# Kernel tuning notes

Measured on AMD Instinct MI355X. Metric: run time of the kernel, lower is better.

Reference implementation:

```python
import jax, jax.numpy as jnp
import numpy as np

N_HEADS = 16
GROUP_SIZE = 4
D_MODEL = 2048
N_GROUPS = N_HEADS // GROUP_SIZE  # 4 KV heads
HEAD_DIM = D_MODEL // N_HEADS     # 128
B, S = 2, 2048


def setup_inputs() -> dict:
    key = jax.random.key(0)
    ks = jax.random.split(key, 10)
    sd = 1.0 / np.sqrt(D_MODEL)
    inp = {
        "x": jax.random.normal(ks[0], (B, S, D_MODEL), dtype=jnp.float32),
        # per-position, per-pair rotation angles (llama-style freqs)
        "rotary_freqs": jax.random.uniform(ks[1], (S, HEAD_DIM // 2), dtype=jnp.float32) * 6.283,
        # weights stored as [in, out] so forward is x @ W + b
        "Wq": jax.random.normal(ks[2], (D_MODEL, D_MODEL), dtype=jnp.float32) * sd,
        "bq": jnp.zeros((D_MODEL,), dtype=jnp.float32),
        "Wk": jax.random.normal(ks[3], (D_MODEL, N_GROUPS * HEAD_DIM), dtype=jnp.float32) * sd,
        "bk": jnp.zeros((N_GROUPS * HEAD_DIM,), dtype=jnp.float32),
        "Wv": jax.random.normal(ks[4], (D_MODEL, N_GROUPS * HEAD_DIM), dtype=jnp.float32) * sd,
        "bv": jnp.zeros((N_GROUPS * HEAD_DIM,), dtype=jnp.float32),
        "Wo": jax.random.normal(ks[5], (D_MODEL, D_MODEL), dtype=jnp.float32) * sd,
        "bo": jnp.zeros((D_MODEL,), dtype=jnp.float32),
    }
    return inp


def _rope(t, cos, sin):
    # t: [B, S, H, head_dim]; cos/sin: [1, S, 1, head_dim//2]
    t2 = t.reshape(t.shape[:-1] + (HEAD_DIM // 2, 2))
    te, to = t2[..., 0], t2[..., 1]
    re = te * cos - to * sin
    ro = te * sin + to * cos
    return jnp.stack([re, ro], axis=-1).reshape(t.shape)


def reference(x, rotary_freqs, Wq, bq, Wk, bk, Wv, bv, Wo, bo):
    Bx, Sx, _ = x.shape
    q = (x @ Wq + bq).reshape(Bx, Sx, N_HEADS, HEAD_DIM)
    k = (x @ Wk + bk).reshape(Bx, Sx, N_GROUPS, HEAD_DIM)
    v = (x @ Wv + bv).reshape(Bx, Sx, N_GROUPS, HEAD_DIM)

    cos = jnp.cos(rotary_freqs)[None, :, None, :]
    sin = jnp.sin(rotary_freqs)[None, :, None, :]
    q = _rope(q, cos, sin)
    k = _rope(k, cos, sin)

    q = q.transpose(0, 2, 1, 3)  # [B, H, S, hd]
    k = k.transpose(0, 2, 1, 3)  # [B, G, S, hd]
    v = v.transpose(0, 2, 1, 3)  # [B, G, S, hd]

    rep = N_HEADS // N_GROUPS
    k = jnp.repeat(k, rep, axis=1)  # repeat_interleave over head dim
    v = jnp.repeat(v, rep, axis=1)

    scores = jnp.einsum("bhsd,bhtd->bhst", q, k) / jnp.sqrt(jnp.float32(HEAD_DIM))
    att = jax.nn.softmax(scores, axis=-1)
    out = jnp.einsum("bhst,bhtd->bhsd", att, v)  # [B, H, S, hd]
    out = out.transpose(0, 2, 1, 3).reshape(Bx, Sx, D_MODEL)
    return out @ Wo + bo
```

## Files before the change

### kernel.cpp

```cpp
#include <hip/hip_runtime.h>
#include <cstdint>
#include <cstddef>

#define NB 2
#define SEQ 2048
#define DMODEL 2048
#define NHEAD 16
#define HDIM 128
#define NGRP 4
#define NKV (NGRP * HDIM)
#define NQKV (DMODEL + 2 * NKV)
#define MROWS (NB * SEQ)
#define QSCALE_LOG2E 0.12751743f

typedef unsigned short u16_t;
typedef unsigned int u32_t;
typedef __bf16 bf16x8 __attribute__((ext_vector_type(8)));
typedef __bf16 bf16x4 __attribute__((ext_vector_type(4)));
typedef float f32x4 __attribute__((ext_vector_type(4)));

static __device__ __forceinline__ u16_t f2bf(float f) {
  u32_t u = __builtin_bit_cast(u32_t, f);
  u32_t r = u + 0x7FFFu + ((u >> 16) & 1u);
  return (u16_t)(r >> 16);
}


__global__ void k_cast_x(const float* __restrict__ x, u16_t* __restrict__ xb) {
  int i = blockIdx.x * 256 + threadIdx.x;
  float4 v = ((const float4*)x)[i];
  uint2 pk;
  pk.x = (u32_t)f2bf(v.x) | ((u32_t)f2bf(v.y) << 16);
  pk.y = (u32_t)f2bf(v.z) | ((u32_t)f2bf(v.w) << 16);
  ((uint2*)xb)[i] = pk;
}

__global__ void k_tables(const float* __restrict__ rf, float* __restrict__ cosT,
                         float* __restrict__ sinT) {
  int i = blockIdx.x * 256 + threadIdx.x;
  float f = rf[i];
  cosT[i] = cosf(f);
  sinT[i] = sinf(f);
}

__global__ void k_bias(const float* __restrict__ bq, const float* __restrict__ bk,
                       const float* __restrict__ bv, float* __restrict__ bqkv) {
  int i = blockIdx.x * 256 + threadIdx.x;
  float v = (i < DMODEL) ? bq[i] : (i < DMODEL + NKV ? bk[i - DMODEL] : bv[i - DMODEL - NKV]);
  bqkv[i] = v;
}

__global__ void k_transpose_cast(const float* __restrict__ W, int N,
                                 u16_t* __restrict__ Wt, int K) {
  __shared__ float tile[64][65];
  int n0 = blockIdx.x * 64, k0 = blockIdx.y * 64;
  int t = threadIdx.x;
#pragma unroll
  for (int pass = 0; pass < 4; ++pass) {
    int slot = pass * 256 + t;
    int r = slot >> 4, c4 = (slot & 15) * 4;
    float4 v = *(const float4*)(W + (size_t)(k0 + r) * N + n0 + c4);
    tile[r][c4] = v.x; tile[r][c4 + 1] = v.y; tile[r][c4 + 2] = v.z; tile[r][c4 + 3] = v.w;
  }
  __syncthreads();
  int nr = t >> 2, seg = t & 3;
  alignas(16) u16_t o[16];
#pragma unroll
  for (int kk = 0; kk < 16; ++kk) o[kk] = f2bf(tile[seg * 16 + kk][nr]);
  u16_t* dst = Wt + (size_t)(n0 + nr) * K + k0 + seg * 16;
  ((int4*)dst)[0] = ((const int4*)o)[0];
  ((int4*)dst)[1] = ((const int4*)o)[1];
}


template <int EPI>
__global__ __launch_bounds__(256, 2) void k_gemm(
    const u16_t* __restrict__ A, const u16_t* __restrict__ Bt, const float* __restrict__ bias,
    float* __restrict__ Cout, u16_t* __restrict__ Qb, u16_t* __restrict__ Kb,
    u16_t* __restrict__ Vt, const float* __restrict__ cosT, const float* __restrict__ sinT,
    int M, int N, int K) {
  __shared__ u16_t lds[16384];
  int tid = threadIdx.x;
  int wid = tid >> 6, lane = tid & 63;
  int l15 = lane & 15, l4 = lane >> 4;
  int wrow = wid >> 1, wcol = wid & 1;

  int m0 = blockIdx.y << 7, n0 = blockIdx.x << 7;

  f32x4 acc[4][4] = {};

  auto stage = [&](int t) {
    u16_t* Al = lds + (t & 1) * 4096;
    u16_t* Bl = lds + 8192 + (t & 1) * 4096;
    int kbase = t * 32;
#pragma unroll
    for (int ss = 0; ss < 2; ++ss) {
      int slot = tid + ss * 256;
      int row = slot >> 2, c = slot & 3;
      int cs = c ^ (row & 3);
      __builtin_amdgcn_global_load_lds(
          (const __attribute__((address_space(1))) u32_t*)(A + (size_t)(m0 + row) * K + kbase + cs * 8),
          (__attribute__((address_space(3))) u32_t*)(Al + slot * 8), 16, 0, 0);
      __builtin_amdgcn_global_load_lds(
          (const __attribute__((address_space(1))) u32_t*)(Bt + (size_t)(n0 + row) * K + kbase + cs * 8),
          (__attribute__((address_space(3))) u32_t*)(Bl + slot * 8), 16, 0, 0);
    }
  };

  stage(0);
  stage(1);

  const int NT = K >> 5;
  for (int t = 0; t < NT; ++t) {
    if (t == NT - 1) {
      asm volatile("s_waitcnt vmcnt(0)" ::: "memory");
    } else {
      asm volatile("s_waitcnt vmcnt(4)" ::: "memory");
    }
    __builtin_amdgcn_s_barrier();
    __builtin_amdgcn_sched_barrier(0);

    const u16_t* Acur = lds + (t & 1) * 4096;
    const u16_t* Bcur = lds + 8192 + (t & 1) * 4096;

    int chunk = l4 ^ (l15 & 3);
    bf16x8 af[4], bfr[4];
#pragma unroll
    for (int i = 0; i < 4; ++i)
      af[i] = *(const bf16x8*)(Acur + (wrow * 64 + i * 16 + l15) * 32 + chunk * 8);
#pragma unroll
    for (int j = 0; j < 4; ++j)
      bfr[j] = *(const bf16x8*)(Bcur + (wcol * 64 + j * 16 + l15) * 32 + chunk * 8);

    __builtin_amdgcn_s_setprio(1);
#pragma unroll
    for (int i = 0; i < 4; ++i)
#pragma unroll
      for (int j = 0; j < 4; ++j)
        acc[i][j] = __builtin_amdgcn_mfma_f32_16x16x32_bf16(af[i], bfr[j], acc[i][j], 0, 0, 0);
    __builtin_amdgcn_s_setprio(0);

    __builtin_amdgcn_sched_barrier(0);
    __builtin_amdgcn_s_barrier();
    __builtin_amdgcn_sched_barrier(0);
    if (t + 2 < NT) stage(t + 2);
  }

  if (EPI == 0) {
#pragma unroll
    for (int j = 0; j < 4; ++j) {
      int n = n0 + wcol * 64 + j * 16 + l15;
      float bs = bias[n];
#pragma unroll
      for (int i = 0; i < 4; ++i) {
        int mbase = m0 + wrow * 64 + i * 16 + l4 * 4;
#pragma unroll
        for (int r = 0; r < 4; ++r)
          Cout[(size_t)(mbase + r) * N + n] = acc[i][j][r] + bs;
      }
    }
  } else {
    bool isV = (n0 >= DMODEL + NKV);
    bool isK = (n0 >= DMODEL) && !isV;
#pragma unroll
    for (int j = 0; j < 4; ++j) {
      int n = n0 + wcol * 64 + j * 16 + l15;
      float bs = bias[n];
      int d = n & (HDIM - 1);
      int p = d >> 1;
      bool evn = !(d & 1);
#pragma unroll
      for (int i = 0; i < 4; ++i) {
        int mbase = m0 + wrow * 64 + i * 16 + l4 * 4;
        if (isV) {
          int g = (n - DMODEL - NKV) >> 7;
          int b = mbase >> 11, s0 = mbase & (SEQ - 1);
          u16_t o[4];
#pragma unroll
          for (int r = 0; r < 4; ++r) o[r] = f2bf(acc[i][j][r] + bs);
          uint2 pk;
          pk.x = (u32_t)o[0] | ((u32_t)o[1] << 16);
          pk.y = (u32_t)o[2] | ((u32_t)o[3] << 16);
          *(uint2*)(Vt + ((size_t)(b * NGRP + g) * HDIM + d) * SEQ + s0) = pk;
        } else {
#pragma unroll
          for (int r = 0; r < 4; ++r) {
            int m = mbase + r;
            int b = m >> 11, s = m & (SEQ - 1);
            float val = acc[i][j][r] + bs;
            float pv = __shfl_xor(val, 1);
            float c = cosT[s * (HDIM / 2) + p];
            float sn = sinT[s * (HDIM / 2) + p];
            float outv = evn ? (val * c - pv * sn) : (pv * sn + val * c);
            if (isK) {
              int g = (n - DMODEL) >> 7;
              Kb[((size_t)(b * NGRP + g) * SEQ + s) * HDIM + d] = f2bf(outv);
            } else {
              int h = n >> 7;
              Qb[((size_t)(b * NHEAD + h) * SEQ + s) * HDIM + d] = f2bf(outv * QSCALE_LOG2E);
            }
          }
        }
      }
    }
  }
}


__global__ __launch_bounds__(256, 2) void k_attn(
    const u16_t* __restrict__ Qb, const u16_t* __restrict__ Kb, const u16_t* __restrict__ Vt,
    u16_t* __restrict__ attn_out) {
  __shared__ u16_t lds[32768];

  int tid = threadIdx.x, wid = tid >> 6, lane = tid & 63;
  int l15 = lane & 15, l4 = lane >> 4;
  int bh = blockIdx.y;
  int b = bh >> 4, h = bh & 15, g = h >> 2;
  int q0 = blockIdx.x * 128;
  const u16_t* Qhead = Qb + (size_t)(b * NHEAD + h) * SEQ * HDIM;
  const u16_t* Khead = Kb + (size_t)(b * NGRP + g) * SEQ * HDIM;
  const u16_t* Vhead = Vt + (size_t)(b * NGRP + g) * HDIM * SEQ;

  bf16x8 qfa[4], qfb[4];
#pragma unroll
  for (int kc = 0; kc < 4; ++kc) {
    qfa[kc] = *(const bf16x8*)(Qhead + (size_t)(q0 + wid * 32 + l15) * HDIM + kc * 32 + l4 * 8);
    qfb[kc] = *(const bf16x8*)(Qhead + (size_t)(q0 + wid * 32 + 16 + l15) * HDIM + kc * 32 + l4 * 8);
  }

  f32x4 oa[8] = {}, ob[8] = {};
  float la = 0.f, lb = 0.f;

  auto stage = [&](int kv0, int bufIdx) {
    u16_t* Kl = lds + bufIdx * 8192;
    u16_t* Vl = lds + 16384 + bufIdx * 8192;
#pragma unroll
    for (int ss = 0; ss < 4; ++ss) {
      int slot = tid + ss * 256;
      int rK = slot >> 4;
      int cK = (slot & 15) ^ ((rK & 3) | (((rK >> 3) & 1) << 2));
      __builtin_amdgcn_global_load_lds(
          (const __attribute__((address_space(1))) u32_t*)(Khead + (size_t)(kv0 + rK) * HDIM + cK * 8),
          (__attribute__((address_space(3))) u32_t*)(Kl + slot * 8), 16, 0, 0);
      int rV = slot >> 3, cV = (slot & 7) ^ (rV & 7);
      __builtin_amdgcn_global_load_lds(
          (const __attribute__((address_space(1))) u32_t*)(Vhead + (size_t)rV * SEQ + kv0 + cV * 8),
          (__attribute__((address_space(3))) u32_t*)(Vl + slot * 8), 16, 0, 0);
    }
  };

  auto qk = [&](int bufIdx, f32x4 (&Sa)[4], f32x4 (&Sb)[4]) {
    const u16_t* Kcur = lds + bufIdx * 8192;
#pragma unroll
    for (int kc = 0; kc < 4; ++kc) {
#pragma unroll
      for (int kvb = 0; kvb < 4; ++kvb) {
        int row = (l15 >> 2) * 8 + ((kvb & 1) << 2) + (l15 & 3) + ((kvb >> 1) << 5);
        int chunk = ((kc << 2) + l4) ^ (l15 & 7);
        bf16x8 kf = *(const bf16x8*)(Kcur + row * 128 + chunk * 8);
        Sa[kvb] = __builtin_amdgcn_mfma_f32_16x16x32_bf16(kf, qfa[kc], Sa[kvb], 0, 0, 0);
        Sb[kvb] = __builtin_amdgcn_mfma_f32_16x16x32_bf16(kf, qfb[kc], Sb[kvb], 0, 0, 0);
      }
    }
  };

  auto expand = [&](f32x4 (&Sa)[4], f32x4 (&Sb)[4], bf16x8 (&pfa)[2], bf16x8 (&pfb)[2]) {
    bf16x4 pa[4], pb[4];
#pragma unroll
    for (int kvb = 0; kvb < 4; ++kvb) {
#pragma unroll
      for (int r = 0; r < 4; ++r) {
        float ea = __builtin_amdgcn_exp2f(Sa[kvb][r]);
        float eb = __builtin_amdgcn_exp2f(Sb[kvb][r]);
        la += ea; lb += eb;
        pa[kvb][r] = (__bf16)ea;
        pb[kvb][r] = (__bf16)eb;
      }
    }
#pragma unroll
    for (int kc2 = 0; kc2 < 2; ++kc2) {
      uint2 alo = __builtin_bit_cast(uint2, pa[kc2 * 2]);
      uint2 ahi = __builtin_bit_cast(uint2, pa[kc2 * 2 + 1]);
      uint4 wa; wa.x = alo.x; wa.y = alo.y; wa.z = ahi.x; wa.w = ahi.y;
      pfa[kc2] = __builtin_bit_cast(bf16x8, wa);
      uint2 blo = __builtin_bit_cast(uint2, pb[kc2 * 2]);
      uint2 bhi = __builtin_bit_cast(uint2, pb[kc2 * 2 + 1]);
      uint4 wb; wb.x = blo.x; wb.y = blo.y; wb.z = bhi.x; wb.w = bhi.y;
      pfb[kc2] = __builtin_bit_cast(bf16x8, wb);
    }
  };

  auto pv = [&](int bufIdx, bf16x8 (&pfa)[2], bf16x8 (&pfb)[2]) {
    const u16_t* Vcur = lds + 16384 + bufIdx * 8192;
#pragma unroll
    for (int kc2 = 0; kc2 < 2; ++kc2) {
#pragma unroll
      for (int dcb = 0; dcb < 8; ++dcb) {
        int chunk = ((kc2 << 2) + l4) ^ (l15 & 7);
        bf16x8 vf = *(const bf16x8*)(Vcur + (dcb * 16 + l15) * 64 + chunk * 8);
        oa[dcb] = __builtin_amdgcn_mfma_f32_16x16x32_bf16(vf, pfa[kc2], oa[dcb], 0, 0, 0);
        ob[dcb] = __builtin_amdgcn_mfma_f32_16x16x32_bf16(vf, pfb[kc2], ob[dcb], 0, 0, 0);
      }
    }
  };

  auto step = [&](int t, f32x4 (&Ia)[4], f32x4 (&Ib)[4], f32x4 (&Oa)[4], f32x4 (&Ob)[4]) {
    bf16x8 pfa[2], pfb[2];
    expand(Ia, Ib, pfa, pfb);
    asm volatile("s_waitcnt vmcnt(0)" ::: "memory");
    __builtin_amdgcn_s_barrier();
    __builtin_amdgcn_sched_barrier(0);
#pragma unroll
    for (int z = 0; z < 4; ++z)
#pragma unroll
      for (int r = 0; r < 4; ++r) { Oa[z][r] = 0.f; Ob[z][r] = 0.f; }
    __builtin_amdgcn_s_setprio(1);
    pv(t & 1, pfa, pfb);
    qk((t + 1) & 1, Oa, Ob);
    __builtin_amdgcn_s_setprio(0);
    __builtin_amdgcn_sched_barrier(0);
    __builtin_amdgcn_s_barrier();
    __builtin_amdgcn_sched_barrier(0);
    if (t + 2 < SEQ / 64) stage((t + 2) * 64, t & 1);
  };

  f32x4 sA[4] = {}, sB[4] = {}, tA[4], tB[4];

  stage(0, 0);
  stage(64, 1);
  asm volatile("s_waitcnt vmcnt(8)" ::: "memory");
  __builtin_amdgcn_s_barrier();
  __builtin_amdgcn_sched_barrier(0);
  qk(0, sA, sB);

  for (int p = 0; p < 15; ++p) {
    step(2 * p, sA, sB, tA, tB);
    step(2 * p + 1, tA, tB, sA, sB);
  }
  step(30, sA, sB, tA, tB);
  {
    bf16x8 pfa[2], pfb[2];
    expand(tA, tB, pfa, pfb);
    pv(1, pfa, pfb);
  }

  la += __shfl_xor(la, 16); la += __shfl_xor(la, 32);
  lb += __shfl_xor(lb, 16); lb += __shfl_xor(lb, 32);
  float inva = 1.0f / la, invb = 1.0f / lb;

#pragma unroll
  for (int half = 0; half < 2; ++half) {
    u16_t* Owave = lds + half * 8704 + wid * 2176;
    const f32x4* oacc = half ? ob : oa;
    float inv = half ? invb : inva;
#pragma unroll
    for (int dcb = 0; dcb < 8; ++dcb) {
      bf16x4 ov;
#pragma unroll
      for (int r = 0; r < 4; ++r) ov[r] = (__bf16)(oacc[dcb][r] * inv);
      *(uint2*)(Owave + l15 * 136 + dcb * 16 + l4 * 4) = __builtin_bit_cast(uint2, ov);
    }
#pragma unroll
    for (int pass = 0; pass < 4; ++pass) {
      int rowq = pass * 4 + l4;
      int4 v = *(const int4*)(Owave + rowq * 136 + l15 * 8);
      int s = q0 + wid * 32 + half * 16 + rowq;
      *(int4*)(attn_out + ((size_t)(b * SEQ + s)) * DMODEL + h * HDIM + l15 * 8) = v;
    }
  }
}


extern "C" void kernel_launch(void* const* d_in, const int* in_sizes, int n_in,
                              void* d_out, int out_size, void* d_ws, size_t ws_size,
                              hipStream_t stream) {
  (void)in_sizes; (void)n_in; (void)out_size; (void)ws_size;
  const float* x  = (const float*)d_in[0];
  const float* rf = (const float*)d_in[1];
  const float* Wq = (const float*)d_in[2];
  const float* bq = (const float*)d_in[3];
  const float* Wk = (const float*)d_in[4];
  const float* bk = (const float*)d_in[5];
  const float* Wv = (const float*)d_in[6];
  const float* bv = (const float*)d_in[7];
  const float* Wo = (const float*)d_in[8];
  const float* bo = (const float*)d_in[9];
  float* out = (float*)d_out;

  char* ws = (char*)d_ws;
  u16_t* xb    = (u16_t*)ws;  ws += (size_t)MROWS * DMODEL * 2;
  u16_t* Wqkvt = (u16_t*)ws;  ws += (size_t)NQKV * DMODEL * 2;
  u16_t* Wot   = (u16_t*)ws;  ws += (size_t)DMODEL * DMODEL * 2;
  float* bqkv  = (float*)ws;  ws += (size_t)NQKV * 4;
  float* cosT  = (float*)ws;  ws += (size_t)SEQ * (HDIM / 2) * 4;
  float* sinT  = (float*)ws;  ws += (size_t)SEQ * (HDIM / 2) * 4;
  u16_t* Qb    = (u16_t*)ws;  ws += (size_t)NB * NHEAD * SEQ * HDIM * 2;
  u16_t* Kb    = (u16_t*)ws;  ws += (size_t)NB * NGRP * SEQ * HDIM * 2;
  u16_t* Vt    = (u16_t*)ws;  ws += (size_t)NB * NGRP * HDIM * SEQ * 2;
  u16_t* attn  = xb;

  k_cast_x<<<MROWS * DMODEL / 1024, 256, 0, stream>>>(x, xb);
  k_tables<<<SEQ * (HDIM / 2) / 256, 256, 0, stream>>>(rf, cosT, sinT);
  k_bias<<<NQKV / 256, 256, 0, stream>>>(bq, bk, bv, bqkv);

  dim3 tgq(DMODEL / 64, DMODEL / 64);
  dim3 tgk(NKV / 64, DMODEL / 64);
  k_transpose_cast<<<tgq, 256, 0, stream>>>(Wq, DMODEL, Wqkvt, DMODEL);
  k_transpose_cast<<<tgk, 256, 0, stream>>>(Wk, NKV, Wqkvt + (size_t)DMODEL * DMODEL, DMODEL);
  k_transpose_cast<<<tgk, 256, 0, stream>>>(Wv, NKV, Wqkvt + (size_t)(DMODEL + NKV) * DMODEL, DMODEL);
  k_transpose_cast<<<tgq, 256, 0, stream>>>(Wo, DMODEL, Wot, DMODEL);

  k_gemm<1><<<dim3(NQKV / 128, MROWS / 128), 256, 0, stream>>>(
      xb, Wqkvt, bqkv, nullptr, Qb, Kb, Vt, cosT, sinT, MROWS, NQKV, DMODEL);

  dim3 ga(SEQ / 128, NB * NHEAD);
  k_attn<<<ga, 256, 0, stream>>>(Qb, Kb, Vt, attn);

  k_gemm<0><<<dim3(DMODEL / 128, MROWS / 128), 256, 0, stream>>>(
      attn, Wot, bo, out, nullptr, nullptr, nullptr, nullptr, nullptr, MROWS, DMODEL, DMODEL);
}
```

Baseline: 206.3 us.

## Double-buffer GEMM fragments in registers to overlap LDS reads with MFMA

Restructures the bf16 GEMM main loop so the next K-tile's LDS fragments are read into a second register set while the current tile's 16 MFMAs issue. The loop is unrolled by two, alternating between the two fragment buffers. The hand-tuned partial vmcnt waits and paired s_barriers are replaced by plain __syncthreads. This adds register pressure. The full-drain barriers may also shorten how long global-to-LDS prefetches stay in flight.

```diff
diff --git a/kernel.cpp b/kernel.cpp
--- a/kernel.cpp
+++ b/kernel.cpp
@@ -107,31 +107,21 @@
     }
   };
 
-  stage(0);
-  stage(1);
-
-  const int NT = K >> 5;
-  for (int t = 0; t < NT; ++t) {
-    if (t == NT - 1) {
-      asm volatile("s_waitcnt vmcnt(0)" ::: "memory");
-    } else {
-      asm volatile("s_waitcnt vmcnt(4)" ::: "memory");
-    }
-    __builtin_amdgcn_s_barrier();
-    __builtin_amdgcn_sched_barrier(0);
-
-    const u16_t* Acur = lds + (t & 1) * 4096;
-    const u16_t* Bcur = lds + 8192 + (t & 1) * 4096;
-
+  auto rdfrags = [&](int t, bf16x8 (&af)[4], bf16x8 (&bfr)[4]) {
+    const u16_t* Ac = lds + (t & 1) * 4096;
+    const u16_t* Bc = lds + 8192 + (t & 1) * 4096;
     int chunk = l4 ^ (l15 & 3);
-    bf16x8 af[4], bfr[4];
 #pragma unroll
     for (int i = 0; i < 4; ++i)
-      af[i] = *(const bf16x8*)(Acur + (wrow * 64 + i * 16 + l15) * 32 + chunk * 8);
+      af[i] = *(const bf16x8*)(Ac + (wrow * 64 + i * 16 + l15) * 32 + chunk * 8);
 #pragma unroll
     for (int j = 0; j < 4; ++j)
-      bfr[j] = *(const bf16x8*)(Bcur + (wcol * 64 + j * 16 + l15) * 32 + chunk * 8);
-
+      bfr[j] = *(const bf16x8*)(Bc + (wcol * 64 + j * 16 + l15) * 32 + chunk * 8);
+  };
+
+  bf16x8 afA[4], bfA[4], afB[4], bfB[4];
+
+  auto mfma16 = [&](bf16x8 (&af)[4], bf16x8 (&bfr)[4]) {
     __builtin_amdgcn_s_setprio(1);
 #pragma unroll
     for (int i = 0; i < 4; ++i)
@@ -139,12 +129,32 @@
       for (int j = 0; j < 4; ++j)
         acc[i][j] = __builtin_amdgcn_mfma_f32_16x16x32_bf16(af[i], bfr[j], acc[i][j], 0, 0, 0);
     __builtin_amdgcn_s_setprio(0);
-
-    __builtin_amdgcn_sched_barrier(0);
-    __builtin_amdgcn_s_barrier();
-    __builtin_amdgcn_sched_barrier(0);
-    if (t + 2 < NT) stage(t + 2);
-  }
+  };
+
+  const int NT = K >> 5;
+
+  stage(0);
+  stage(1);
+  __syncthreads();
+  rdfrags(0, afA, bfA);
+  __syncthreads();
+
+  for (int p = 0; p < NT / 2 - 1; ++p) {
+    int t0 = 2 * p;
+    if (t0 + 2 < NT) stage(t0 + 2);
+    rdfrags(t0 + 1, afB, bfB);
+    mfma16(afA, bfA);
+    __syncthreads();
+    int t1 = 2 * p + 1;
+    if (t1 + 2 < NT) stage(t1 + 2);
+    rdfrags(t1 + 1, afA, bfA);
+    mfma16(afB, bfB);
+    __syncthreads();
+  }
+  rdfrags(NT - 1, afB, bfB);
+  mfma16(afA, bfA);
+  __syncthreads();
+  mfma16(afB, bfB);
 
   if (EPI == 0) {
 #pragma unroll
```

Result: faster. 199.2 us (-3.4%).

## Triple-buffer GEMM LDS tiles and prefetch next fragments during MFMA

Applied to the files above, without the earlier changes.

Moves the GEMM k-loop from double to triple LDS buffering and issues the global-to-LDS load for tile t+2 before the MFMAs of tile t. Register fragments for tile t+1 are read from LDS while the MFMAs for tile t run, using ping-pong fragment registers. The aim is to hide both global load latency and LDS read latency behind matrix math. In exchange it uses more LDS per block (48KB) and more VGPRs, which could reduce occupancy under the 2-block launch bound.

```diff
diff --git a/kernel.cpp b/kernel.cpp
--- a/kernel.cpp
+++ b/kernel.cpp
@@ -79,7 +79,7 @@
     float* __restrict__ Cout, u16_t* __restrict__ Qb, u16_t* __restrict__ Kb,
     u16_t* __restrict__ Vt, const float* __restrict__ cosT, const float* __restrict__ sinT,
     int M, int N, int K) {
-  __shared__ u16_t lds[16384];
+  __shared__ u16_t lds[24576];
   int tid = threadIdx.x;
   int wid = tid >> 6, lane = tid & 63;
   int l15 = lane & 15, l4 = lane >> 4;
@@ -90,8 +90,9 @@
   f32x4 acc[4][4] = {};
 
   auto stage = [&](int t) {
-    u16_t* Al = lds + (t & 1) * 4096;
-    u16_t* Bl = lds + 8192 + (t & 1) * 4096;
+    int slot3 = t % 3;
+    u16_t* Al = lds + slot3 * 4096;
+    u16_t* Bl = lds + 12288 + slot3 * 4096;
     int kbase = t * 32;
 #pragma unroll
     for (int ss = 0; ss < 2; ++ss) {
@@ -107,31 +108,22 @@
     }
   };
 
-  stage(0);
-  stage(1);
-
-  const int NT = K >> 5;
-  for (int t = 0; t < NT; ++t) {
-    if (t == NT - 1) {
-      asm volatile("s_waitcnt vmcnt(0)" ::: "memory");
-    } else {
-      asm volatile("s_waitcnt vmcnt(4)" ::: "memory");
-    }
-    __builtin_amdgcn_s_barrier();
-    __builtin_amdgcn_sched_barrier(0);
-
-    const u16_t* Acur = lds + (t & 1) * 4096;
-    const u16_t* Bcur = lds + 8192 + (t & 1) * 4096;
-
+  auto rdfrags = [&](int t, bf16x8 (&af)[4], bf16x8 (&bfr)[4]) {
+    int slot3 = t % 3;
+    const u16_t* Ac = lds + slot3 * 4096;
+    const u16_t* Bc = lds + 12288 + slot3 * 4096;
     int chunk = l4 ^ (l15 & 3);
-    bf16x8 af[4], bfr[4];
 #pragma unroll
     for (int i = 0; i < 4; ++i)
-      af[i] = *(const bf16x8*)(Acur + (wrow * 64 + i * 16 + l15) * 32 + chunk * 8);
+      af[i] = *(const bf16x8*)(Ac + (wrow * 64 + i * 16 + l15) * 32 + chunk * 8);
 #pragma unroll
     for (int j = 0; j < 4; ++j)
-      bfr[j] = *(const bf16x8*)(Bcur + (wcol * 64 + j * 16 + l15) * 32 + chunk * 8);
-
+      bfr[j] = *(const bf16x8*)(Bc + (wcol * 64 + j * 16 + l15) * 32 + chunk * 8);
+  };
+
+  bf16x8 afA[4], bfA[4], afB[4], bfB[4];
+
+  auto mfma16 = [&](bf16x8 (&af)[4], bf16x8 (&bfr)[4]) {
     __builtin_amdgcn_s_setprio(1);
 #pragma unroll
     for (int i = 0; i < 4; ++i)
@@ -139,11 +131,37 @@
       for (int j = 0; j < 4; ++j)
         acc[i][j] = __builtin_amdgcn_mfma_f32_16x16x32_bf16(af[i], bfr[j], acc[i][j], 0, 0, 0);
     __builtin_amdgcn_s_setprio(0);
-
-    __builtin_amdgcn_sched_barrier(0);
+  };
+
+  const int NT = K >> 5;
+
+  auto region = [&](int t, bf16x8 (&aC)[4], bf16x8 (&bC)[4],
+                    bf16x8 (&aN)[4], bf16x8 (&bN)[4]) {
+    if (t + 2 < NT) {
+      stage(t + 2);
+      asm volatile("s_waitcnt vmcnt(4)" ::: "memory");
+    } else {
+      asm volatile("s_waitcnt vmcnt(0)" ::: "memory");
+    }
     __builtin_amdgcn_s_barrier();
     __builtin_amdgcn_sched_barrier(0);
-    if (t + 2 < NT) stage(t + 2);
+    if (t + 1 < NT) rdfrags(t + 1, aN, bN);
+    mfma16(aC, bC);
+    __builtin_amdgcn_sched_barrier(0);
+    __builtin_amdgcn_s_barrier();
+    __builtin_amdgcn_sched_barrier(0);
+  };
+
+  stage(0);
+  stage(1);
+  asm volatile("s_waitcnt vmcnt(4)" ::: "memory");
+  __builtin_amdgcn_s_barrier();
+  __builtin_amdgcn_sched_barrier(0);
+  rdfrags(0, afA, bfA);
+
+  for (int pp = 0; pp < NT / 2; ++pp) {
+    region(2 * pp, afA, bfA, afB, bfB);
+    region(2 * pp + 1, afB, bfB, afA, bfA);
   }
 
   if (EPI == 0) {
```

After: 206.6 us. About the same (+0.2%).
